# Performance work log

Hardware: AMD Instinct MI355X
Metric: run time of the kernel (lower is better)

Reference implementation:

```python
import jax, jax.numpy as jnp
import numpy as np

N_NODES = 100000
N_EDGES = 640000
D = 128


def setup_inputs() -> dict:
    key = jax.random.key(0)
    k1, k2, k3 = jax.random.split(key, 3)
    x = jax.random.normal(k1, (N_NODES, D), dtype=jnp.float32)
    W = jax.random.normal(k2, (D, D), dtype=jnp.float32) * (1.0 / np.sqrt(D))
    edge_index = jax.random.randint(k3, (2, N_EDGES), 0, N_NODES, dtype=jnp.int64)
    return {"x": x, "W": W, "edge_index": edge_index}


def reference(x, W, edge_index):
    # Linear (bias-free): x @ W^T matches torch.nn.Linear semantics
    h = jnp.matmul(x, W.T)  # [N, D]
    src, dst = edge_index[0], edge_index[1]
    # message = norm * x_j with norm == 1, aggr='add':
    # out[i] = sum_{(j->i) in E} h[j]
    out = jax.ops.segment_sum(h[src], dst, num_segments=x.shape[0])
    return out
```

## Files before the change

### kernel.cpp

```cpp
#include <hip/hip_runtime.h>
#include <hip/hip_bf16.h>

#define NNODES 100000
#define NEDGES 640000
#define DIM    128
#define CAP    32
#define NCHUNK (NNODES * DIM / 8)

typedef __attribute__((ext_vector_type(8))) __bf16 bf16x8;
typedef __attribute__((ext_vector_type(4))) float  f32x4;

__device__ __forceinline__ uint bf16pair(float a, float b) {
    uint ua = __float_as_uint(a), ub = __float_as_uint(b);
    ua = (ua + 0x7FFFu + ((ua >> 16) & 1u)) >> 16;
    ub = (ub + 0x7FFFu + ((ub >> 16) & 1u)) >> 16;
    return (ub << 16) | (ua & 0xFFFFu);
}

__global__ __launch_bounds__(256) void prep_kernel(
    const float* __restrict__ x, const float* __restrict__ W,
    const int* __restrict__ ei,
    int4* __restrict__ xb4, int4* __restrict__ wb4,
    int* __restrict__ cursor, int* __restrict__ csr)
{
    int id = blockIdx.x * 256 + threadIdx.x;
    const float4* p = reinterpret_cast<const float4*>(x) + (size_t)id * 2;
    float4 f0 = p[0], f1 = p[1];
    int4 v = {(int)bf16pair(f0.x, f0.y), (int)bf16pair(f0.z, f0.w),
              (int)bf16pair(f1.x, f1.y), (int)bf16pair(f1.z, f1.w)};
    xb4[id] = v;
    if (id < 2048) {
        const float4* q = reinterpret_cast<const float4*>(W) + (size_t)id * 2;
        float4 g0 = q[0], g1 = q[1];
        int4 wv = {(int)bf16pair(g0.x, g0.y), (int)bf16pair(g0.z, g0.w),
                   (int)bf16pair(g1.x, g1.y), (int)bf16pair(g1.z, g1.w)};
        wb4[id] = wv;
    }
    if (id < NEDGES) {
        int src = ei[id];
        int dst = ei[NEDGES + id];
        int pos = atomicAdd(&cursor[dst], 1);
        if (pos < CAP) csr[dst * CAP + pos] = src;
    }
}

__global__ __launch_bounds__(256) void gather_kernel(
    const int2* __restrict__ xb, const int* __restrict__ cursor,
    const int* __restrict__ csr, float* out)
{
    int node = blockIdx.x * 8 + (threadIdx.x >> 5);
    int lane = threadIdx.x & 31;
    int cnt = cursor[node];
    if (cnt > CAP) cnt = CAP;
    const int* lst = csr + (size_t)node * CAP;
    float4 acc = {0.f, 0.f, 0.f, 0.f}, acc2 = {0.f, 0.f, 0.f, 0.f};
    int j = 0;
    for (; j + 1 < cnt; j += 2) {
        int2 v0 = xb[(size_t)lst[j] * 32 + lane];
        int2 v1 = xb[(size_t)lst[j + 1] * 32 + lane];
        acc.x  += __uint_as_float((uint)v0.x << 16);
        acc.y  += __uint_as_float((uint)v0.x & 0xFFFF0000u);
        acc.z  += __uint_as_float((uint)v0.y << 16);
        acc.w  += __uint_as_float((uint)v0.y & 0xFFFF0000u);
        acc2.x += __uint_as_float((uint)v1.x << 16);
        acc2.y += __uint_as_float((uint)v1.x & 0xFFFF0000u);
        acc2.z += __uint_as_float((uint)v1.y << 16);
        acc2.w += __uint_as_float((uint)v1.y & 0xFFFF0000u);
    }
    if (j < cnt) {
        int2 v0 = xb[(size_t)lst[j] * 32 + lane];
        acc.x += __uint_as_float((uint)v0.x << 16);
        acc.y += __uint_as_float((uint)v0.x & 0xFFFF0000u);
        acc.z += __uint_as_float((uint)v0.y << 16);
        acc.w += __uint_as_float((uint)v0.y & 0xFFFF0000u);
    }
    acc.x += acc2.x; acc.y += acc2.y; acc.z += acc2.z; acc.w += acc2.w;
    int2 pk = {(int)bf16pair(acc.x, acc.y), (int)bf16pair(acc.z, acc.w)};
    reinterpret_cast<int2*>((char*)out + (size_t)node * 512 + 256)[lane] = pk;
}

__global__ __launch_bounds__(256) void gemm_mfma(float* out,
                                                 const int4* __restrict__ wb)
{
    __shared__ int4 w_lds[128 * 16];
    __shared__ int4 a_lds[64 * 16];
    int tid = threadIdx.x;
    long base = (long)blockIdx.x * 64;

    for (int i = 0; i < 8; ++i) {
        int c = i * 256 + tid;
        int d = c >> 4, k8 = c & 15;
        w_lds[(c & ~15) | (k8 ^ (d & 7))] = wb[c];
    }
    for (int i = 0; i < 4; ++i) {
        int c = i * 256 + tid;
        int r = c >> 4, k8 = c & 15;
        int4 v = {0, 0, 0, 0};
        long node = base + r;
        if (node < NNODES)
            v = *reinterpret_cast<const int4*>((const char*)out + node * 512 + 256 + k8 * 16);
        a_lds[(c & ~15) | (k8 ^ (r & 7))] = v;
    }
    __syncthreads();

    int l64 = tid & 63;
    int w   = tid >> 6;
    int rl  = l64 & 15;
    int kg  = l64 >> 4;

    f32x4 acc[8] = {};
#pragma unroll
    for (int kc = 0; kc < 4; ++kc) {
        int arow = w * 16 + rl;
        int k8 = kc * 4 + kg;
        int4 araw = a_lds[arow * 16 + (k8 ^ (arow & 7))];
        bf16x8 af = *reinterpret_cast<bf16x8*>(&araw);
#pragma unroll
        for (int dt = 0; dt < 8; ++dt) {
            int d = dt * 16 + rl;
            int4 braw = w_lds[d * 16 + (k8 ^ (d & 7))];
            bf16x8 bf = *reinterpret_cast<bf16x8*>(&braw);
            acc[dt] = __builtin_amdgcn_mfma_f32_16x16x32_bf16(af, bf, acc[dt], 0, 0, 0);
        }
    }
#pragma unroll
    for (int dt = 0; dt < 8; ++dt) {
#pragma unroll
        for (int j = 0; j < 4; ++j) {
            long r = base + w * 16 + kg * 4 + j;
            if (r < NNODES) out[r * DIM + dt * 16 + rl] = acc[dt][j];
        }
    }
}

extern "C" void kernel_launch(void* const* d_in, const int* in_sizes, int n_in,
                              void* d_out, int out_size, void* d_ws, size_t ws_size,
                              hipStream_t stream) {
    const float* x  = (const float*)d_in[0];
    const float* W  = (const float*)d_in[1];
    const int*   ei = (const int*)d_in[2];
    float* out = (float*)d_out;

    int*  cursor = (int*)d_ws;
    int*  csr    = cursor + 100352;
    int4* xb4    = (int4*)(csr + NNODES * CAP);
    int4* wb4    = xb4 + NCHUNK;

    hipMemsetAsync(cursor, 0, (size_t)100352 * sizeof(int), stream);
    prep_kernel<<<NCHUNK / 256, 256, 0, stream>>>(x, W, ei, xb4, wb4, cursor, csr);
    gather_kernel<<<NNODES / 8, 256, 0, stream>>>((const int2*)xb4, cursor, csr, out);
    gemm_mfma<<<(NNODES + 63) / 64, 256, 0, stream>>>(out, wb4);
}
```

Measured before the change: 187.8 us.

## Fuse neighbor gather with MFMA GEMM via LDS and split prep kernel

The gather and GEMM kernels are merged into one 1024-thread block per 32 nodes. Each half-wave aggregates one node's neighbors into swizzled LDS, and then 16 waves each compute a 16x16 output tile with MFMA. This removes the bf16 intermediate round-trip through the output buffer and one kernel launch. The edge-fill and x-cast work is split into separate kernels. Each block reloads the full W tile for only 32 rows, so more LDS traffic per row and larger blocks may lower occupancy.

```diff
diff --git a/kernel.cpp b/kernel.cpp
--- a/kernel.cpp
+++ b/kernel.cpp
@@ -17,12 +17,20 @@
     return (ub << 16) | (ua & 0xFFFFu);
 }
 
-__global__ __launch_bounds__(256) void prep_kernel(
-    const float* __restrict__ x, const float* __restrict__ W,
-    const int* __restrict__ ei,
-    int4* __restrict__ xb4, int4* __restrict__ wb4,
-    int* __restrict__ cursor, int* __restrict__ csr)
-{
+__global__ __launch_bounds__(256) void fill_kernel(const int* __restrict__ ei,
+                                                   int* __restrict__ cursor,
+                                                   int* __restrict__ csr) {
+    int e = blockIdx.x * 256 + threadIdx.x;
+    int src = ei[e];
+    int dst = ei[NEDGES + e];
+    int pos = atomicAdd(&cursor[dst], 1);
+    if (pos < CAP) csr[dst * CAP + pos] = src;
+}
+
+__global__ __launch_bounds__(256) void xcast_kernel(const float* __restrict__ x,
+                                                    const float* __restrict__ W,
+                                                    int4* __restrict__ xb4,
+                                                    int4* __restrict__ wb4) {
     int id = blockIdx.x * 256 + threadIdx.x;
     const float4* p = reinterpret_cast<const float4*>(x) + (size_t)id * 2;
     float4 f0 = p[0], f1 = p[1];
@@ -36,101 +44,79 @@
                    (int)bf16pair(g1.x, g1.y), (int)bf16pair(g1.z, g1.w)};
         wb4[id] = wv;
     }
-    if (id < NEDGES) {
-        int src = ei[id];
-        int dst = ei[NEDGES + id];
-        int pos = atomicAdd(&cursor[dst], 1);
-        if (pos < CAP) csr[dst * CAP + pos] = src;
-    }
 }
 
-__global__ __launch_bounds__(256) void gather_kernel(
-    const int2* __restrict__ xb, const int* __restrict__ cursor,
-    const int* __restrict__ csr, float* out)
-{
-    int node = blockIdx.x * 8 + (threadIdx.x >> 5);
-    int lane = threadIdx.x & 31;
-    int cnt = cursor[node];
-    if (cnt > CAP) cnt = CAP;
-    const int* lst = csr + (size_t)node * CAP;
-    float4 acc = {0.f, 0.f, 0.f, 0.f}, acc2 = {0.f, 0.f, 0.f, 0.f};
-    int j = 0;
-    for (; j + 1 < cnt; j += 2) {
-        int2 v0 = xb[(size_t)lst[j] * 32 + lane];
-        int2 v1 = xb[(size_t)lst[j + 1] * 32 + lane];
-        acc.x  += __uint_as_float((uint)v0.x << 16);
-        acc.y  += __uint_as_float((uint)v0.x & 0xFFFF0000u);
-        acc.z  += __uint_as_float((uint)v0.y << 16);
-        acc.w  += __uint_as_float((uint)v0.y & 0xFFFF0000u);
-        acc2.x += __uint_as_float((uint)v1.x << 16);
-        acc2.y += __uint_as_float((uint)v1.x & 0xFFFF0000u);
-        acc2.z += __uint_as_float((uint)v1.y << 16);
-        acc2.w += __uint_as_float((uint)v1.y & 0xFFFF0000u);
-    }
-    if (j < cnt) {
-        int2 v0 = xb[(size_t)lst[j] * 32 + lane];
-        acc.x += __uint_as_float((uint)v0.x << 16);
-        acc.y += __uint_as_float((uint)v0.x & 0xFFFF0000u);
-        acc.z += __uint_as_float((uint)v0.y << 16);
-        acc.w += __uint_as_float((uint)v0.y & 0xFFFF0000u);
-    }
-    acc.x += acc2.x; acc.y += acc2.y; acc.z += acc2.z; acc.w += acc2.w;
-    int2 pk = {(int)bf16pair(acc.x, acc.y), (int)bf16pair(acc.z, acc.w)};
-    reinterpret_cast<int2*>((char*)out + (size_t)node * 512 + 256)[lane] = pk;
-}
-
-__global__ __launch_bounds__(256) void gemm_mfma(float* out,
-                                                 const int4* __restrict__ wb)
+__global__ __launch_bounds__(1024) void fused_gg(
+    const int2* __restrict__ xb, const int4* __restrict__ wb,
+    const int* __restrict__ cursor, const int* __restrict__ csr,
+    float* __restrict__ out)
 {
     __shared__ int4 w_lds[128 * 16];
-    __shared__ int4 a_lds[64 * 16];
+    __shared__ int4 a_lds[32 * 16];
     int tid = threadIdx.x;
-    long base = (long)blockIdx.x * 64;
+    long base = (long)blockIdx.x * 32;
 
-    for (int i = 0; i < 8; ++i) {
-        int c = i * 256 + tid;
+#pragma unroll
+    for (int i = 0; i < 2; ++i) {
+        int c = i * 1024 + tid;
         int d = c >> 4, k8 = c & 15;
         w_lds[(c & ~15) | (k8 ^ (d & 7))] = wb[c];
     }
-    for (int i = 0; i < 4; ++i) {
-        int c = i * 256 + tid;
-        int r = c >> 4, k8 = c & 15;
-        int4 v = {0, 0, 0, 0};
-        long node = base + r;
-        if (node < NNODES)
-            v = *reinterpret_cast<const int4*>((const char*)out + node * 512 + 256 + k8 * 16);
-        a_lds[(c & ~15) | (k8 ^ (r & 7))] = v;
+
+    int hw = tid >> 5, lane = tid & 31;
+    {
+        long node = base + hw;
+        int cnt = cursor[node];
+        if (cnt > CAP) cnt = CAP;
+        const int* lst = csr + node * CAP;
+        float4 acc = {0.f, 0.f, 0.f, 0.f}, acc2 = {0.f, 0.f, 0.f, 0.f};
+        int j = 0;
+        for (; j + 1 < cnt; j += 2) {
+            int2 v0 = xb[(size_t)lst[j] * 32 + lane];
+            int2 v1 = xb[(size_t)lst[j + 1] * 32 + lane];
+            acc.x  += __uint_as_float((uint)v0.x << 16);
+            acc.y  += __uint_as_float((uint)v0.x & 0xFFFF0000u);
+            acc.z  += __uint_as_float((uint)v0.y << 16);
+            acc.w  += __uint_as_float((uint)v0.y & 0xFFFF0000u);
+            acc2.x += __uint_as_float((uint)v1.x << 16);
+            acc2.y += __uint_as_float((uint)v1.x & 0xFFFF0000u);
+            acc2.z += __uint_as_float((uint)v1.y << 16);
+            acc2.w += __uint_as_float((uint)v1.y & 0xFFFF0000u);
+        }
+        if (j < cnt) {
+            int2 v0 = xb[(size_t)lst[j] * 32 + lane];
+            acc.x += __uint_as_float((uint)v0.x << 16);
+            acc.y += __uint_as_float((uint)v0.x & 0xFFFF0000u);
+            acc.z += __uint_as_float((uint)v0.y << 16);
+            acc.w += __uint_as_float((uint)v0.y & 0xFFFF0000u);
+        }
+        acc.x += acc2.x; acc.y += acc2.y; acc.z += acc2.z; acc.w += acc2.w;
+        int2 pk = {(int)bf16pair(acc.x, acc.y), (int)bf16pair(acc.z, acc.w)};
+        reinterpret_cast<int2*>(a_lds)[hw * 32 + (((lane >> 1) ^ (hw & 7)) << 1) + (lane & 1)] = pk;
     }
     __syncthreads();
 
     int l64 = tid & 63;
     int w   = tid >> 6;
+    int rt  = w >> 3, dt = w & 7;
     int rl  = l64 & 15;
     int kg  = l64 >> 4;
 
-    f32x4 acc[8] = {};
+    f32x4 acc = {};
 #pragma unroll
     for (int kc = 0; kc < 4; ++kc) {
-        int arow = w * 16 + rl;
+        int arow = rt * 16 + rl;
         int k8 = kc * 4 + kg;
         int4 araw = a_lds[arow * 16 + (k8 ^ (arow & 7))];
         bf16x8 af = *reinterpret_cast<bf16x8*>(&araw);
-#pragma unroll
-        for (int dt = 0; dt < 8; ++dt) {
-            int d = dt * 16 + rl;
-            int4 braw = w_lds[d * 16 + (k8 ^ (d & 7))];
-            bf16x8 bf = *reinterpret_cast<bf16x8*>(&braw);
-            acc[dt] = __builtin_amdgcn_mfma_f32_16x16x32_bf16(af, bf, acc[dt], 0, 0, 0);
-        }
+        int d = dt * 16 + rl;
+        int4 braw = w_lds[d * 16 + (k8 ^ (d & 7))];
+        bf16x8 bf = *reinterpret_cast<bf16x8*>(&braw);
+        acc = __builtin_amdgcn_mfma_f32_16x16x32_bf16(af, bf, acc, 0, 0, 0);
     }
 #pragma unroll
-    for (int dt = 0; dt < 8; ++dt) {
-#pragma unroll
-        for (int j = 0; j < 4; ++j) {
-            long r = base + w * 16 + kg * 4 + j;
-            if (r < NNODES) out[r * DIM + dt * 16 + rl] = acc[dt][j];
-        }
-    }
+    for (int j = 0; j < 4; ++j)
+        out[(base + rt * 16 + kg * 4 + j) * DIM + dt * 16 + rl] = acc[j];
 }
 
 extern "C" void kernel_launch(void* const* d_in, const int* in_sizes, int n_in,
@@ -147,7 +133,8 @@
     int4* wb4    = xb4 + NCHUNK;
 
     hipMemsetAsync(cursor, 0, (size_t)100352 * sizeof(int), stream);
-    prep_kernel<<<NCHUNK / 256, 256, 0, stream>>>(x, W, ei, xb4, wb4, cursor, csr);
-    gather_kernel<<<NNODES / 8, 256, 0, stream>>>((const int2*)xb4, cursor, csr, out);
-    gemm_mfma<<<(NNODES + 63) / 64, 256, 0, stream>>>(out, wb4);
+    fill_kernel<<<NEDGES / 256, 256, 0, stream>>>(ei, cursor, csr);
+    xcast_kernel<<<NCHUNK / 256, 256, 0, stream>>>(x, W, xb4, wb4);
+    fused_gg<<<NNODES / 32, 1024, 0, stream>>>(
+        (const int2*)xb4, wb4, cursor, csr, out);
 }
```

Measured after the change: 181.0 us. -3.6%, faster.
